# Kernel tuning notes

Measured on AMD Instinct MI355X. Metric: run time of the kernel, lower is better.

The kernel has to match this reference:

```python
import jax, jax.numpy as jnp
import numpy as np

H = 32  # hidden size (fixed in source)
V = 95  # input_size == output_size == vocab of chars


def _init_param(key, shape, fan):
    bound = 1.0 / np.sqrt(fan)
    return jax.random.uniform(key, shape, dtype=jnp.float32, minval=-bound, maxval=bound)


def setup_inputs() -> dict:
    key = jax.random.key(0)
    ks = jax.random.split(key, 16)
    B, T = 2048, 256
    inp = {"x": jax.random.normal(ks[0], (B, T, V), dtype=jnp.float32)}
    in_sizes = [V, H, H]
    i = 1
    for l, isz in enumerate(in_sizes, start=1):
        inp[f"Wih{l}"] = _init_param(ks[i], (3 * H, isz), H); i += 1
        inp[f"Whh{l}"] = _init_param(ks[i], (3 * H, H), H); i += 1
        inp[f"bih{l}"] = _init_param(ks[i], (3 * H,), H); i += 1
        inp[f"bhh{l}"] = _init_param(ks[i], (3 * H,), H); i += 1
    inp["Wfc"] = _init_param(ks[13], (V, H), H)
    inp["bfc"] = _init_param(ks[14], (V,), H)
    return inp


def gru_layer(x, Wih, Whh, bih, bhh):
    # x: [B, T, I] -> hs: [B, T, H]; PyTorch GRU gate math, h0 = 0.
    B, T, _ = x.shape
    # Precompute input projections for all timesteps (batched GEMM).
    xp = jnp.einsum('bti,gi->btg', x, Wih) + bih          # [B, T, 3H]
    xr, xz, xn = jnp.split(xp, 3, axis=-1)                # each [B, T, H]
    xs = (jnp.swapaxes(xr, 0, 1), jnp.swapaxes(xz, 0, 1), jnp.swapaxes(xn, 0, 1))
    Whr, Whz, Whn = jnp.split(Whh, 3, axis=0)             # each [H, H]
    bhr, bhz, bhn = jnp.split(bhh, 3, axis=0)

    def step(h, t_in):
        txr, txz, txn = t_in
        r = jax.nn.sigmoid(txr + h @ Whr.T + bhr)
        z = jax.nn.sigmoid(txz + h @ Whz.T + bhz)
        n = jnp.tanh(txn + r * (h @ Whn.T + bhn))
        h_new = (1.0 - z) * n + z * h
        return h_new, h_new

    h0 = jnp.zeros((B, Whh.shape[1]), dtype=x.dtype)
    _, hs = jax.lax.scan(step, h0, xs)                    # hs: [T, B, H]
    return jnp.swapaxes(hs, 0, 1)                         # [B, T, H]


def reference(x, Wih1, Whh1, bih1, bhh1, Wih2, Whh2, bih2, bhh2,
              Wih3, Whh3, bih3, bhh3, Wfc, bfc):
    out = gru_layer(x, Wih1, Whh1, bih1, bhh1)
    out = gru_layer(out, Wih2, Whh2, bih2, bhh2)
    out = gru_layer(out, Wih3, Whh3, bih3, bhh3)
    return jnp.einsum('bth,oh->bto', out, Wfc) + bfc      # [B, T, V]
```

## Files before the change

### kernel.cpp

```cpp
#include <hip/hip_runtime.h>

#define HH 32
#define VV 95
#define TT 256

__device__ __forceinline__ float fast_sigmoid(float v) {
    return __builtin_amdgcn_rcpf(1.0f + __expf(-v));
}
__device__ __forceinline__ float fast_tanh(float v) {
    return 1.0f - 2.0f * __builtin_amdgcn_rcpf(__expf(2.0f * v) + 1.0f);
}
__device__ __forceinline__ void wave_fence() {
    asm volatile("s_waitcnt lgkmcnt(0)" ::: "memory");
    __builtin_amdgcn_wave_barrier();
}

extern "C" __global__ void __launch_bounds__(256, 1) gru_l1(
    const float* __restrict__ x,
    const float* __restrict__ Wih1, const float* __restrict__ Whh1,
    const float* __restrict__ bih1, const float* __restrict__ bhh1,
    float* __restrict__ out)
{
    __shared__ float sW[96 * 95];
    __shared__ float xst[2][8][96];
    __shared__ float hb[8][32];

    const int tid = threadIdx.x;
    for (int i = tid; i < 96 * 95; i += 256) sW[i] = Wih1[i];

    const int s = tid >> 5, j = tid & 31;
    float ur[32], uz[32], un[32];
    #pragma unroll
    for (int k = 0; k < 32; ++k) {
        ur[k] = Whh1[j * 32 + k];
        uz[k] = Whh1[(32 + j) * 32 + k];
        un[k] = Whh1[(64 + j) * 32 + k];
    }
    const float bir = bih1[j], biz = bih1[32 + j], bin_ = bih1[64 + j];
    const float bhr = bhh1[j], bhz = bhh1[32 + j], bhn = bhh1[64 + j];

    const size_t b = (size_t)blockIdx.x * 8 + s;
    const float* xrow = x + b * (size_t)(TT * VV);
    float* orow = out + b * (size_t)(TT * VV);

    hb[s][j] = 0.0f;
    float hj = 0.0f;
    for (int i = j; i < VV; i += 32) xst[0][s][i] = xrow[i];
    __syncthreads();

    const float* wr = sW + j * 95;
    const float* wz = sW + (32 + j) * 95;
    const float* wn = sW + (64 + j) * 95;

    for (int t = 0; t < TT; ++t) {
        const int cur = t & 1;
        float p0 = 0.f, p1 = 0.f, p2 = 0.f;
        if (t + 1 < TT) {
            const float* xn_ = xrow + (t + 1) * VV;
            p0 = xn_[j]; p1 = xn_[32 + j];
            p2 = (j < 31) ? xn_[64 + j] : 0.f;
        }
        const float* xs = xst[cur][s];
        float ar = bir, az = biz, an = bin_;
        #pragma unroll
        for (int i4 = 0; i4 < 23; ++i4) {
            const float4 xv = ((const float4*)xs)[i4];
            const int i = i4 * 4;
            ar = fmaf(wr[i    ], xv.x, ar); az = fmaf(wz[i    ], xv.x, az); an = fmaf(wn[i    ], xv.x, an);
            ar = fmaf(wr[i + 1], xv.y, ar); az = fmaf(wz[i + 1], xv.y, az); an = fmaf(wn[i + 1], xv.y, an);
            ar = fmaf(wr[i + 2], xv.z, ar); az = fmaf(wz[i + 2], xv.z, az); an = fmaf(wn[i + 2], xv.z, an);
            ar = fmaf(wr[i + 3], xv.w, ar); az = fmaf(wz[i + 3], xv.w, az); an = fmaf(wn[i + 3], xv.w, an);
        }
        #pragma unroll
        for (int i = 92; i < 95; ++i) {
            const float xi = xs[i];
            ar = fmaf(wr[i], xi, ar); az = fmaf(wz[i], xi, az); an = fmaf(wn[i], xi, an);
        }
        float hr = bhr, hz = bhz, hn = bhn;
        #pragma unroll
        for (int k = 0; k < 32; ++k) {
            const float hk = hb[s][k];
            hr = fmaf(ur[k], hk, hr); hz = fmaf(uz[k], hk, hz); hn = fmaf(un[k], hk, hn);
        }
        const float r = fast_sigmoid(ar + hr);
        const float z = fast_sigmoid(az + hz);
        const float n = fast_tanh(an + r * hn);
        hj = (1.0f - z) * n + z * hj;

        asm volatile("" ::: "memory");
        hb[s][j] = hj;
        orow[t * 95 + j] = hj;
        if (t + 1 < TT) {
            float* xd = xst[cur ^ 1][s];
            xd[j] = p0; xd[32 + j] = p1;
            if (j < 31) xd[64 + j] = p2;
        }
        wave_fence();
    }
}

extern "C" __global__ void __launch_bounds__(256, 1) gru_l2(
    const float* __restrict__ Wih2, const float* __restrict__ Whh2,
    const float* __restrict__ bih2, const float* __restrict__ bhh2,
    float* __restrict__ out)
{
    __shared__ float ist[2][8][32];
    __shared__ float hb[8][32];
    const int tid = threadIdx.x;
    const int s = tid >> 5, j = tid & 31;

    float vr[32], vz[32], vn[32], ur[32], uz[32], un[32];
    #pragma unroll
    for (int k = 0; k < 32; ++k) {
        vr[k] = Wih2[j * 32 + k];        vz[k] = Wih2[(32 + j) * 32 + k];  vn[k] = Wih2[(64 + j) * 32 + k];
        ur[k] = Whh2[j * 32 + k];        uz[k] = Whh2[(32 + j) * 32 + k];  un[k] = Whh2[(64 + j) * 32 + k];
    }
    const float bir = bih2[j], biz = bih2[32 + j], bin_ = bih2[64 + j];
    const float bhr = bhh2[j], bhz = bhh2[32 + j], bhn = bhh2[64 + j];

    const size_t b = (size_t)blockIdx.x * 8 + s;
    float* orow = out + b * (size_t)(TT * VV);

    hb[s][j] = 0.0f;
    float hj = 0.0f;
    ist[0][s][j] = orow[j];
    wave_fence();

    for (int t = 0; t < TT; ++t) {
        const int cur = t & 1;
        float pn = 0.f;
        if (t + 1 < TT) pn = orow[(t + 1) * 95 + j];

        const float* in = ist[cur][s];
        float ar = bir, az = biz, an = bin_;
        float hr = bhr, hz = bhz, hn = bhn;
        #pragma unroll
        for (int k = 0; k < 32; ++k) {
            const float ik = in[k], hk = hb[s][k];
            ar = fmaf(vr[k], ik, ar); az = fmaf(vz[k], ik, az); an = fmaf(vn[k], ik, an);
            hr = fmaf(ur[k], hk, hr); hz = fmaf(uz[k], hk, hz); hn = fmaf(un[k], hk, hn);
        }
        const float r = fast_sigmoid(ar + hr);
        const float z = fast_sigmoid(az + hz);
        const float n = fast_tanh(an + r * hn);
        hj = (1.0f - z) * n + z * hj;

        orow[t * 95 + 32 + j] = hj;
        asm volatile("" ::: "memory");
        hb[s][j] = hj;
        if (t + 1 < TT) ist[cur ^ 1][s][j] = pn;
        wave_fence();
    }
}

extern "C" __global__ void __launch_bounds__(256, 1) gru_l3fc(
    const float* __restrict__ Wih3, const float* __restrict__ Whh3,
    const float* __restrict__ bih3, const float* __restrict__ bhh3,
    const float* __restrict__ Wfc,  const float* __restrict__ bfc,
    float* __restrict__ out)
{
    __shared__ float ist[2][8][32];
    __shared__ float hb[8][32];
    const int tid = threadIdx.x;
    const int s = tid >> 5, j = tid & 31;

    float vr[32], vz[32], vn[32], ur[32], uz[32], un[32];
    float wf0[32], wf1[32], wf2[32];
    #pragma unroll
    for (int k = 0; k < 32; ++k) {
        vr[k] = Wih3[j * 32 + k];        vz[k] = Wih3[(32 + j) * 32 + k];  vn[k] = Wih3[(64 + j) * 32 + k];
        ur[k] = Whh3[j * 32 + k];        uz[k] = Whh3[(32 + j) * 32 + k];  un[k] = Whh3[(64 + j) * 32 + k];
        wf0[k] = Wfc[j * 32 + k];
        wf1[k] = Wfc[(32 + j) * 32 + k];
        wf2[k] = (j < 31) ? Wfc[(64 + j) * 32 + k] : 0.f;
    }
    const float bir = bih3[j], biz = bih3[32 + j], bin_ = bih3[64 + j];
    const float bhr = bhh3[j], bhz = bhh3[32 + j], bhn = bhh3[64 + j];
    const float bf0 = bfc[j], bf1 = bfc[32 + j], bf2 = (j < 31) ? bfc[64 + j] : 0.f;

    const size_t b = (size_t)blockIdx.x * 8 + s;
    float* orow = out + b * (size_t)(TT * VV);

    hb[s][j] = 0.0f;
    float hj = 0.0f;
    ist[0][s][j] = orow[32 + j];
    wave_fence();

    for (int t = 0; t < TT; ++t) {
        const int cur = t & 1;
        float pn = 0.f;
        if (t + 1 < TT) pn = orow[(t + 1) * 95 + 32 + j];

        const float* in = ist[cur][s];
        float ar = bir, az = biz, an = bin_;
        float hr = bhr, hz = bhz, hn = bhn;
        #pragma unroll
        for (int k = 0; k < 32; ++k) {
            const float ik = in[k], hk = hb[s][k];
            ar = fmaf(vr[k], ik, ar); az = fmaf(vz[k], ik, az); an = fmaf(vn[k], ik, an);
            hr = fmaf(ur[k], hk, hr); hz = fmaf(uz[k], hk, hz); hn = fmaf(un[k], hk, hn);
        }
        const float r = fast_sigmoid(ar + hr);
        const float z = fast_sigmoid(az + hz);
        const float n = fast_tanh(an + r * hn);
        hj = (1.0f - z) * n + z * hj;

        asm volatile("" ::: "memory");
        hb[s][j] = hj;
        wave_fence();

        float o0 = bf0, o1 = bf1, o2 = bf2;
        #pragma unroll
        for (int k = 0; k < 32; ++k) {
            const float hk = hb[s][k];
            o0 = fmaf(wf0[k], hk, o0); o1 = fmaf(wf1[k], hk, o1); o2 = fmaf(wf2[k], hk, o2);
        }
        float* op = orow + t * 95;
        op[j] = o0; op[32 + j] = o1;
        if (j < 31) op[64 + j] = o2;

        asm volatile("" ::: "memory");
        if (t + 1 < TT) ist[cur ^ 1][s][j] = pn;
        wave_fence();
    }
}

extern "C" void kernel_launch(void* const* d_in, const int* in_sizes, int n_in,
                              void* d_out, int out_size, void* d_ws, size_t ws_size,
                              hipStream_t stream) {
    const float* x    = (const float*)d_in[0];
    const float* Wih1 = (const float*)d_in[1];
    const float* Whh1 = (const float*)d_in[2];
    const float* bih1 = (const float*)d_in[3];
    const float* bhh1 = (const float*)d_in[4];
    const float* Wih2 = (const float*)d_in[5];
    const float* Whh2 = (const float*)d_in[6];
    const float* bih2 = (const float*)d_in[7];
    const float* bhh2 = (const float*)d_in[8];
    const float* Wih3 = (const float*)d_in[9];
    const float* Whh3 = (const float*)d_in[10];
    const float* bih3 = (const float*)d_in[11];
    const float* bhh3 = (const float*)d_in[12];
    const float* Wfc  = (const float*)d_in[13];
    const float* bfc  = (const float*)d_in[14];
    float* out = (float*)d_out;

    dim3 grid(256), block(256);
    hipLaunchKernelGGL(gru_l1, grid, block, 0, stream, x, Wih1, Whh1, bih1, bhh1, out);
    hipLaunchKernelGGL(gru_l2, grid, block, 0, stream, Wih2, Whh2, bih2, bhh2, out);
    hipLaunchKernelGGL(gru_l3fc, grid, block, 0, stream, Wih3, Whh3, bih3, bhh3, Wfc, bfc, out);
}
```

Before: 1.054 ms.

## Precompute layer-1 input projection as GEMM and fuse three GRU layers in wavefront pipeline

```diff
diff --git a/kernel.cpp b/kernel.cpp
--- a/kernel.cpp
+++ b/kernel.cpp
@@ -1,8 +1,7 @@
 #include <hip/hip_runtime.h>
 
-#define HH 32
+#define TT 256
 #define VV 95
-#define TT 256
 
 __device__ __forceinline__ float fast_sigmoid(float v) {
     return __builtin_amdgcn_rcpf(1.0f + __expf(-v));
@@ -10,218 +9,268 @@
 __device__ __forceinline__ float fast_tanh(float v) {
     return 1.0f - 2.0f * __builtin_amdgcn_rcpf(__expf(2.0f * v) + 1.0f);
 }
-__device__ __forceinline__ void wave_fence() {
+__device__ __forceinline__ void block_sync_lds() {
     asm volatile("s_waitcnt lgkmcnt(0)" ::: "memory");
-    __builtin_amdgcn_wave_barrier();
-}
-
-extern "C" __global__ void __launch_bounds__(256, 1) gru_l1(
+    __builtin_amdgcn_s_barrier();
+}
+
+__device__ __forceinline__ float dot16(const float* w, float4 a, float4 b, float4 c, float4 d) {
+    float s = 0.0f;
+    s = fmaf(w[0],  a.x, s); s = fmaf(w[1],  a.y, s); s = fmaf(w[2],  a.z, s); s = fmaf(w[3],  a.w, s);
+    s = fmaf(w[4],  b.x, s); s = fmaf(w[5],  b.y, s); s = fmaf(w[6],  b.z, s); s = fmaf(w[7],  b.w, s);
+    s = fmaf(w[8],  c.x, s); s = fmaf(w[9],  c.y, s); s = fmaf(w[10], c.z, s); s = fmaf(w[11], c.w, s);
+    s = fmaf(w[12], d.x, s); s = fmaf(w[13], d.y, s); s = fmaf(w[14], d.z, s); s = fmaf(w[15], d.w, s);
+    return s;
+}
+
+__global__ void __launch_bounds__(256) k0_xproj(
+    const float* __restrict__ x, const float* __restrict__ Wih1,
+    const float* __restrict__ bih1, float* __restrict__ out)
+{
+    __shared__ float xs[64 * 100];
+    __shared__ float ws[96 * 100];
+    const int tid = threadIdx.x;
+    const size_t row0 = (size_t)blockIdx.x * 64;
+
+    const float* xg = x + row0 * VV;
+    for (int i = tid; i < 64 * VV; i += 256) {
+        const int r = i / VV, c = i - r * VV;
+        xs[r * 100 + c] = xg[i];
+    }
+    for (int i = tid; i < 96 * VV; i += 256) {
+        const int g = i / VV, c = i - g * VV;
+        ws[g * 100 + c] = Wih1[i];
+    }
+    for (int i = tid; i < 64 * 5; i += 256) xs[(i / 5) * 100 + 95 + (i % 5)] = 0.f;
+    for (int i = tid; i < 96 * 5; i += 256) ws[(i / 5) * 100 + 95 + (i % 5)] = 0.f;
+
+    const int cq = tid & 15, rq = tid >> 4;
+    float acc[4][6];
+    #pragma unroll
+    for (int c = 0; c < 6; ++c) {
+        const float bv = bih1[cq + 16 * c];
+        acc[0][c] = bv; acc[1][c] = bv; acc[2][c] = bv; acc[3][c] = bv;
+    }
+    __syncthreads();
+
+    const float* xp0 = xs + rq * 100;
+    const float* wp0 = ws + cq * 100;
+    #pragma unroll 4
+    for (int k4 = 0; k4 < 24; ++k4) {
+        const int k = k4 * 4;
+        float4 xv0 = *(const float4*)(xp0 + k);
+        float4 xv1 = *(const float4*)(xp0 + 1600 + k);
+        float4 xv2 = *(const float4*)(xp0 + 3200 + k);
+        float4 xv3 = *(const float4*)(xp0 + 4800 + k);
+        #pragma unroll
+        for (int c = 0; c < 6; ++c) {
+            const float4 wv = *(const float4*)(wp0 + c * 1600 + k);
+            acc[0][c] = fmaf(xv0.x, wv.x, acc[0][c]); acc[0][c] = fmaf(xv0.y, wv.y, acc[0][c]);
+            acc[0][c] = fmaf(xv0.z, wv.z, acc[0][c]); acc[0][c] = fmaf(xv0.w, wv.w, acc[0][c]);
+            acc[1][c] = fmaf(xv1.x, wv.x, acc[1][c]); acc[1][c] = fmaf(xv1.y, wv.y, acc[1][c]);
+            acc[1][c] = fmaf(xv1.z, wv.z, acc[1][c]); acc[1][c] = fmaf(xv1.w, wv.w, acc[1][c]);
+            acc[2][c] = fmaf(xv2.x, wv.x, acc[2][c]); acc[2][c] = fmaf(xv2.y, wv.y, acc[2][c]);
+            acc[2][c] = fmaf(xv2.z, wv.z, acc[2][c]); acc[2][c] = fmaf(xv2.w, wv.w, acc[2][c]);
+            acc[3][c] = fmaf(xv3.x, wv.x, acc[3][c]); acc[3][c] = fmaf(xv3.y, wv.y, acc[3][c]);
+            acc[3][c] = fmaf(xv3.z, wv.z, acc[3][c]); acc[3][c] = fmaf(xv3.w, wv.w, acc[3][c]);
+        }
+    }
+    #pragma unroll
+    for (int r = 0; r < 4; ++r) {
+        float* orow = out + (row0 + rq + 16 * r) * VV;
+        #pragma unroll
+        for (int c = 0; c < 6; ++c) {
+            const int g = cq + 16 * c;
+            if (g < VV) orow[g] = acc[r][c];
+        }
+    }
+}
+
+extern "C" __global__ void __launch_bounds__(256) gru_fused(
     const float* __restrict__ x,
     const float* __restrict__ Wih1, const float* __restrict__ Whh1,
     const float* __restrict__ bih1, const float* __restrict__ bhh1,
-    float* __restrict__ out)
-{
-    __shared__ float sW[96 * 95];
-    __shared__ float xst[2][8][96];
-    __shared__ float hb[8][32];
-
-    const int tid = threadIdx.x;
-    for (int i = tid; i < 96 * 95; i += 256) sW[i] = Wih1[i];
-
-    const int s = tid >> 5, j = tid & 31;
-    float ur[32], uz[32], un[32];
-    #pragma unroll
-    for (int k = 0; k < 32; ++k) {
-        ur[k] = Whh1[j * 32 + k];
-        uz[k] = Whh1[(32 + j) * 32 + k];
-        un[k] = Whh1[(64 + j) * 32 + k];
-    }
-    const float bir = bih1[j], biz = bih1[32 + j], bin_ = bih1[64 + j];
-    const float bhr = bhh1[j], bhz = bhh1[32 + j], bhn = bhh1[64 + j];
-
-    const size_t b = (size_t)blockIdx.x * 8 + s;
-    const float* xrow = x + b * (size_t)(TT * VV);
-    float* orow = out + b * (size_t)(TT * VV);
-
-    hb[s][j] = 0.0f;
-    float hj = 0.0f;
-    for (int i = j; i < VV; i += 32) xst[0][s][i] = xrow[i];
-    __syncthreads();
-
-    const float* wr = sW + j * 95;
-    const float* wz = sW + (32 + j) * 95;
-    const float* wn = sW + (64 + j) * 95;
-
-    for (int t = 0; t < TT; ++t) {
-        const int cur = t & 1;
-        float p0 = 0.f, p1 = 0.f, p2 = 0.f;
-        if (t + 1 < TT) {
-            const float* xn_ = xrow + (t + 1) * VV;
-            p0 = xn_[j]; p1 = xn_[32 + j];
-            p2 = (j < 31) ? xn_[64 + j] : 0.f;
-        }
-        const float* xs = xst[cur][s];
-        float ar = bir, az = biz, an = bin_;
-        #pragma unroll
-        for (int i4 = 0; i4 < 23; ++i4) {
-            const float4 xv = ((const float4*)xs)[i4];
-            const int i = i4 * 4;
-            ar = fmaf(wr[i    ], xv.x, ar); az = fmaf(wz[i    ], xv.x, az); an = fmaf(wn[i    ], xv.x, an);
-            ar = fmaf(wr[i + 1], xv.y, ar); az = fmaf(wz[i + 1], xv.y, az); an = fmaf(wn[i + 1], xv.y, an);
-            ar = fmaf(wr[i + 2], xv.z, ar); az = fmaf(wz[i + 2], xv.z, az); an = fmaf(wn[i + 2], xv.z, an);
-            ar = fmaf(wr[i + 3], xv.w, ar); az = fmaf(wz[i + 3], xv.w, az); an = fmaf(wn[i + 3], xv.w, an);
-        }
-        #pragma unroll
-        for (int i = 92; i < 95; ++i) {
-            const float xi = xs[i];
-            ar = fmaf(wr[i], xi, ar); az = fmaf(wz[i], xi, az); an = fmaf(wn[i], xi, an);
-        }
-        float hr = bhr, hz = bhz, hn = bhn;
-        #pragma unroll
-        for (int k = 0; k < 32; ++k) {
-            const float hk = hb[s][k];
-            hr = fmaf(ur[k], hk, hr); hz = fmaf(uz[k], hk, hz); hn = fmaf(un[k], hk, hn);
-        }
-        const float r = fast_sigmoid(ar + hr);
-        const float z = fast_sigmoid(az + hz);
-        const float n = fast_tanh(an + r * hn);
-        hj = (1.0f - z) * n + z * hj;
-
-        asm volatile("" ::: "memory");
-        hb[s][j] = hj;
-        orow[t * 95 + j] = hj;
-        if (t + 1 < TT) {
-            float* xd = xst[cur ^ 1][s];
-            xd[j] = p0; xd[32 + j] = p1;
-            if (j < 31) xd[64 + j] = p2;
-        }
-        wave_fence();
-    }
-}
-
-extern "C" __global__ void __launch_bounds__(256, 1) gru_l2(
     const float* __restrict__ Wih2, const float* __restrict__ Whh2,
     const float* __restrict__ bih2, const float* __restrict__ bhh2,
-    float* __restrict__ out)
-{
-    __shared__ float ist[2][8][32];
-    __shared__ float hb[8][32];
-    const int tid = threadIdx.x;
-    const int s = tid >> 5, j = tid & 31;
-
-    float vr[32], vz[32], vn[32], ur[32], uz[32], un[32];
-    #pragma unroll
-    for (int k = 0; k < 32; ++k) {
-        vr[k] = Wih2[j * 32 + k];        vz[k] = Wih2[(32 + j) * 32 + k];  vn[k] = Wih2[(64 + j) * 32 + k];
-        ur[k] = Whh2[j * 32 + k];        uz[k] = Whh2[(32 + j) * 32 + k];  un[k] = Whh2[(64 + j) * 32 + k];
-    }
-    const float bir = bih2[j], biz = bih2[32 + j], bin_ = bih2[64 + j];
-    const float bhr = bhh2[j], bhz = bhh2[32 + j], bhn = bhh2[64 + j];
-
-    const size_t b = (size_t)blockIdx.x * 8 + s;
-    float* orow = out + b * (size_t)(TT * VV);
-
-    hb[s][j] = 0.0f;
-    float hj = 0.0f;
-    ist[0][s][j] = orow[j];
-    wave_fence();
-
-    for (int t = 0; t < TT; ++t) {
-        const int cur = t & 1;
-        float pn = 0.f;
-        if (t + 1 < TT) pn = orow[(t + 1) * 95 + j];
-
-        const float* in = ist[cur][s];
-        float ar = bir, az = biz, an = bin_;
-        float hr = bhr, hz = bhz, hn = bhn;
-        #pragma unroll
-        for (int k = 0; k < 32; ++k) {
-            const float ik = in[k], hk = hb[s][k];
-            ar = fmaf(vr[k], ik, ar); az = fmaf(vz[k], ik, az); an = fmaf(vn[k], ik, an);
-            hr = fmaf(ur[k], hk, hr); hz = fmaf(uz[k], hk, hz); hn = fmaf(un[k], hk, hn);
-        }
-        const float r = fast_sigmoid(ar + hr);
-        const float z = fast_sigmoid(az + hz);
-        const float n = fast_tanh(an + r * hn);
-        hj = (1.0f - z) * n + z * hj;
-
-        orow[t * 95 + 32 + j] = hj;
-        asm volatile("" ::: "memory");
-        hb[s][j] = hj;
-        if (t + 1 < TT) ist[cur ^ 1][s][j] = pn;
-        wave_fence();
-    }
-}
-
-extern "C" __global__ void __launch_bounds__(256, 1) gru_l3fc(
     const float* __restrict__ Wih3, const float* __restrict__ Whh3,
     const float* __restrict__ bih3, const float* __restrict__ bhh3,
     const float* __restrict__ Wfc,  const float* __restrict__ bfc,
     float* __restrict__ out)
 {
-    __shared__ float ist[2][8][32];
-    __shared__ float hb[8][32];
+    __shared__ __align__(16) float hbuf[3][2][32];
+    __shared__ float xn31[2];
+
+    float (*h1b)[32] = hbuf[0];
+    float (*h2b)[32] = hbuf[1];
+    float (*h3b)[32] = hbuf[2];
+
     const int tid = threadIdx.x;
-    const int s = tid >> 5, j = tid & 31;
-
-    float vr[32], vz[32], vn[32], ur[32], uz[32], un[32];
-    float wf0[32], wf1[32], wf2[32];
-    #pragma unroll
-    for (int k = 0; k < 32; ++k) {
-        vr[k] = Wih3[j * 32 + k];        vz[k] = Wih3[(32 + j) * 32 + k];  vn[k] = Wih3[(64 + j) * 32 + k];
-        ur[k] = Whh3[j * 32 + k];        uz[k] = Whh3[(32 + j) * 32 + k];  un[k] = Whh3[(64 + j) * 32 + k];
-        wf0[k] = Wfc[j * 32 + k];
-        wf1[k] = Wfc[(32 + j) * 32 + k];
-        wf2[k] = (j < 31) ? Wfc[(64 + j) * 32 + k] : 0.f;
-    }
-    const float bir = bih3[j], biz = bih3[32 + j], bin_ = bih3[64 + j];
-    const float bhr = bhh3[j], bhz = bhh3[32 + j], bhn = bhh3[64 + j];
-    const float bf0 = bfc[j], bf1 = bfc[32 + j], bf2 = (j < 31) ? bfc[64 + j] : 0.f;
-
-    const size_t b = (size_t)blockIdx.x * 8 + s;
+    const int w = tid >> 6, l = tid & 63, j = l & 31, p = l >> 5;
+
+    const size_t b = blockIdx.x;
+    const float* xrow = x + b * (size_t)(TT * VV);
     float* orow = out + b * (size_t)(TT * VV);
 
-    hb[s][j] = 0.0f;
-    float hj = 0.0f;
-    ist[0][s][j] = orow[32 + j];
-    wave_fence();
-
-    for (int t = 0; t < TT; ++t) {
-        const int cur = t & 1;
-        float pn = 0.f;
-        if (t + 1 < TT) pn = orow[(t + 1) * 95 + 32 + j];
-
-        const float* in = ist[cur][s];
-        float ar = bir, az = biz, an = bin_;
-        float hr = bhr, hz = bhz, hn = bhn;
-        #pragma unroll
-        for (int k = 0; k < 32; ++k) {
-            const float ik = in[k], hk = hb[s][k];
-            ar = fmaf(vr[k], ik, ar); az = fmaf(vz[k], ik, az); an = fmaf(vn[k], ik, an);
-            hr = fmaf(ur[k], hk, hr); hz = fmaf(uz[k], hk, hz); hn = fmaf(un[k], hk, hn);
-        }
-        const float r = fast_sigmoid(ar + hr);
-        const float z = fast_sigmoid(az + hz);
-        const float n = fast_tanh(an + r * hn);
-        hj = (1.0f - z) * n + z * hj;
-
-        asm volatile("" ::: "memory");
-        hb[s][j] = hj;
-        wave_fence();
-
-        float o0 = bf0, o1 = bf1, o2 = bf2;
-        #pragma unroll
-        for (int k = 0; k < 32; ++k) {
-            const float hk = hb[s][k];
-            o0 = fmaf(wf0[k], hk, o0); o1 = fmaf(wf1[k], hk, o1); o2 = fmaf(wf2[k], hk, o2);
-        }
-        float* op = orow + t * 95;
-        op[j] = o0; op[32 + j] = o1;
-        if (j < 31) op[64 + j] = o2;
-
-        asm volatile("" ::: "memory");
-        if (t + 1 < TT) ist[cur ^ 1][s][j] = pn;
-        wave_fence();
+    if (tid < 192) (&hbuf[0][0][0])[tid] = 0.f;
+
+    float wr_[16], wz_[16], wn_[16], ur_[16], uz_[16], un_[16];
+    float br = 0.f, bz = 0.f, bni = 0.f, bnh = 0.f;
+    float wa = 0.f, wb = 0.f, bn95 = 0.f;
+    const int i0 = 2 * l, i1 = 2 * l + 1;
+
+    if (w == 0) {
+        #pragma unroll
+        for (int c = 0; c < 16; ++c) {
+            ur_[c] = Whh1[j * 32 + 16 * p + c];
+            uz_[c] = Whh1[(32 + j) * 32 + 16 * p + c];
+            un_[c] = Whh1[(64 + j) * 32 + 16 * p + c];
+        }
+        br = bhh1[j]; bz = bhh1[32 + j]; bnh = bhh1[64 + j];
+    } else if (w == 3) {
+        #pragma unroll
+        for (int c = 0; c < 16; ++c) {
+            wr_[c] = Wfc[j * 32 + 16 * p + c];
+            wz_[c] = Wfc[(32 + j) * 32 + 16 * p + c];
+            wn_[c] = (j < 31) ? Wfc[(64 + j) * 32 + 16 * p + c] : 0.f;
+        }
+        br = bfc[j]; bz = bfc[32 + j]; bni = (j < 31) ? bfc[64 + j] : 0.f;
+        wa = (i0 < VV) ? Wih1[95 * VV + i0] : 0.f;
+        wb = (i1 < VV) ? Wih1[95 * VV + i1] : 0.f;
+        bn95 = bih1[95];
+    } else {
+        const float* Wih_ = (w == 1) ? Wih2 : Wih3;
+        const float* Whh_ = (w == 1) ? Whh2 : Whh3;
+        const float* bih_ = (w == 1) ? bih2 : bih3;
+        const float* bhh_ = (w == 1) ? bhh2 : bhh3;
+        #pragma unroll
+        for (int c = 0; c < 16; ++c) {
+            wr_[c] = Wih_[j * 32 + 16 * p + c];
+            wz_[c] = Wih_[(32 + j) * 32 + 16 * p + c];
+            wn_[c] = Wih_[(64 + j) * 32 + 16 * p + c];
+            ur_[c] = Whh_[j * 32 + 16 * p + c];
+            uz_[c] = Whh_[(32 + j) * 32 + 16 * p + c];
+            un_[c] = Whh_[(64 + j) * 32 + 16 * p + c];
+        }
+        br = bih_[j] + bhh_[j];
+        bz = bih_[32 + j] + bhh_[32 + j];
+        bni = bih_[64 + j]; bnh = bhh_[64 + j];
+    }
+
+    float (*inB)[32]  = (w == 1) ? h1b : h2b;
+    float (*ownB)[32] = (w == 1) ? h2b : h3b;
+
+    float AxR = 0.f, AxZ = 0.f, AxN = 0.f, BxR = 0.f, BxZ = 0.f, BxN = 0.f;
+    float xaA = 0.f, xbA = 0.f, xaB = 0.f, xbB = 0.f;
+    float hj = 0.f;
+
+    if (w == 0 && p == 0) {
+        AxR = orow[j]; AxZ = orow[32 + j]; AxN = (j < 31) ? orow[64 + j] : 0.f;
+        const float* r1 = orow + VV;
+        BxR = r1[j]; BxZ = r1[32 + j]; BxN = (j < 31) ? r1[64 + j] : 0.f;
+    }
+    if (w == 3) {
+        float a0v = (i0 < VV) ? xrow[i0] : 0.f;
+        float b0v = (i1 < VV) ? xrow[i1] : 0.f;
+        float v0 = fmaf(wa, a0v, wb * b0v);
+        v0 += __shfl_xor(v0, 1);  v0 += __shfl_xor(v0, 2);  v0 += __shfl_xor(v0, 4);
+        v0 += __shfl_xor(v0, 8);  v0 += __shfl_xor(v0, 16); v0 += __shfl_xor(v0, 32);
+        if (l == 0) xn31[0] = v0 + bn95;
+        const float* x1 = xrow + 1 * VV;
+        const float* x2 = xrow + 2 * VV;
+        xaB = (i0 < VV) ? x1[i0] : 0.f; xbB = (i1 < VV) ? x1[i1] : 0.f;
+        xaA = (i0 < VV) ? x2[i0] : 0.f; xbA = (i1 < VV) ? x2[i1] : 0.f;
+    }
+    __syncthreads();
+
+    for (int g = 0; g < TT + 3; ++g) {
+        const int par = g & 1, prv = par ^ 1;
+        if (w == 0) {
+            if (g < TT) {
+                const float xr = (par == 0) ? AxR : BxR;
+                const float xz = (par == 0) ? AxZ : BxZ;
+                const float xn = (par == 0) ? AxN : BxN;
+                const float4* hv = (const float4*)(&h1b[prv][16 * p]);
+                const float4 h0 = hv[0], h1v = hv[1], h2v = hv[2], h3v = hv[3];
+                float hr = dot16(ur_, h0, h1v, h2v, h3v);
+                float hz = dot16(uz_, h0, h1v, h2v, h3v);
+                float hn = dot16(un_, h0, h1v, h2v, h3v);
+                hr += __shfl_xor(hr, 32);
+                hz += __shfl_xor(hz, 32);
+                hn += __shfl_xor(hn, 32);
+                const float xnf = (j == 31) ? xn31[par] : xn;
+                const float r = fast_sigmoid(xr + hr + br);
+                const float z = fast_sigmoid(xz + hz + bz);
+                const float n = fast_tanh(xnf + r * (hn + bnh));
+                hj = (1.0f - z) * n + z * hj;
+                if (p == 0) {
+                    h1b[par][j] = hj;
+                    if (g + 2 < TT) {
+                        const float* nx = orow + (g + 2) * VV;
+                        const float nr = nx[j], nz = nx[32 + j];
+                        const float nn = (j < 31) ? nx[64 + j] : 0.f;
+                        if (par == 0) { AxR = nr; AxZ = nz; AxN = nn; }
+                        else          { BxR = nr; BxZ = nz; BxN = nn; }
+                    }
+                }
+            }
+        } else if (w == 3) {
+            if (g >= 3) {
+                const int t3 = g - 3;
+                const float4* gv = (const float4*)(&h3b[t3 & 1][16 * p]);
+                const float4 g0 = gv[0], g1 = gv[1], g2 = gv[2], g3 = gv[3];
+                float o0 = dot16(wr_, g0, g1, g2, g3);
+                float o1 = dot16(wz_, g0, g1, g2, g3);
+                float o2 = dot16(wn_, g0, g1, g2, g3);
+                o0 += __shfl_xor(o0, 32);
+                o1 += __shfl_xor(o1, 32);
+                o2 += __shfl_xor(o2, 32);
+                if (p == 0) {
+                    float* op = orow + t3 * VV;
+                    op[j] = o0 + br;
+                    op[32 + j] = o1 + bz;
+                    if (j < 31) op[64 + j] = o2 + bni;
+                }
+            }
+            if (g + 1 < TT) {
+                const float xa = (prv == 0) ? xaA : xaB;
+                const float xb = (prv == 0) ? xbA : xbB;
+                float v = fmaf(wa, xa, wb * xb);
+                v += __shfl_xor(v, 1);  v += __shfl_xor(v, 2);  v += __shfl_xor(v, 4);
+                v += __shfl_xor(v, 8);  v += __shfl_xor(v, 16); v += __shfl_xor(v, 32);
+                if (l == 0) xn31[prv] = v + bn95;
+                if (g + 3 < TT) {
+                    const float* xx = xrow + (g + 3) * VV;
+                    const float na = (i0 < VV) ? xx[i0] : 0.f;
+                    const float nb = (i1 < VV) ? xx[i1] : 0.f;
+                    if (prv == 0) { xaA = na; xbA = nb; }
+                    else          { xaB = na; xbB = nb; }
+                }
+            }
+        } else {
+            if (g >= w && g < TT + w) {
+                const int slot = (g - w) & 1;
+                const float4* iv = (const float4*)(&inB[slot][16 * p]);
+                const float4 a0 = iv[0], a1 = iv[1], a2 = iv[2], a3 = iv[3];
+                const float4* hv = (const float4*)(&ownB[slot ^ 1][16 * p]);
+                const float4 h0 = hv[0], h1v = hv[1], h2v = hv[2], h3v = hv[3];
+                float ar = dot16(wr_, a0, a1, a2, a3);
+                float az = dot16(wz_, a0, a1, a2, a3);
+                float an = dot16(wn_, a0, a1, a2, a3);
+                float hr = dot16(ur_, h0, h1v, h2v, h3v);
+                float hz = dot16(uz_, h0, h1v, h2v, h3v);
+                float hn = dot16(un_, h0, h1v, h2v, h3v);
+                float s1 = ar + hr; s1 += __shfl_xor(s1, 32);
+                float s2 = az + hz; s2 += __shfl_xor(s2, 32);
+                an += __shfl_xor(an, 32);
+                hn += __shfl_xor(hn, 32);
+                const float r = fast_sigmoid(s1 + br);
+                const float z = fast_sigmoid(s2 + bz);
+                const float n = fast_tanh(an + bni + r * (hn + bnh));
+                hj = (1.0f - z) * n + z * hj;
+                if (p == 0) ownB[slot][j] = hj;
+            }
+        }
+        block_sync_lds();
     }
 }
 
@@ -245,8 +294,10 @@
     const float* bfc  = (const float*)d_in[14];
     float* out = (float*)d_out;
 
-    dim3 grid(256), block(256);
-    hipLaunchKernelGGL(gru_l1, grid, block, 0, stream, x, Wih1, Whh1, bih1, bhh1, out);
-    hipLaunchKernelGGL(gru_l2, grid, block, 0, stream, Wih2, Whh2, bih2, bhh2, out);
-    hipLaunchKernelGGL(gru_l3fc, grid, block, 0, stream, Wih3, Whh3, bih3, bhh3, Wfc, bfc, out);
-}
+    hipLaunchKernelGGL(k0_xproj, dim3(8192), dim3(256), 0, stream, x, Wih1, bih1, out);
+    hipLaunchKernelGGL(gru_fused, dim3(2048), dim3(256), 0, stream,
+                       x, Wih1, Whh1, bih1, bhh1,
+                       Wih2, Whh2, bih2, bhh2,
+                       Wih3, Whh3, bih3, bhh3,
+                       Wfc, bfc, out);
+}
```

Result: slower. 1.497 ms (+42.1%).
